# Optimization experiments

Measured on AMD Instinct MI355X. Metric: run time of the kernel, lower is better.

The kernel has to match this reference:

```python
import jax, jax.numpy as jnp
import numpy as np

N_NODES = 50000
N_EDGES = 800000
D = 128
H = 128


def setup_inputs() -> dict:
    key = jax.random.key(0)
    ks = jax.random.split(key, 8)
    s = 1.0 / np.sqrt(D)
    return {
        "x": jax.random.normal(ks[0], (N_NODES, D), dtype=jnp.float32),
        "edge_index": jax.random.randint(ks[1], (2, N_EDGES), 0, N_NODES, dtype=jnp.int64),
        "W1_l": jax.random.normal(ks[2], (D, H), dtype=jnp.float32) * s,
        "b1_l": jax.random.normal(ks[3], (H,), dtype=jnp.float32) * s,
        "W1_r": jax.random.normal(ks[4], (D, H), dtype=jnp.float32) * s,
        "W2_l": jax.random.normal(ks[5], (H, H), dtype=jnp.float32) * s,
        "b2_l": jax.random.normal(ks[6], (H,), dtype=jnp.float32) * s,
        "W2_r": jax.random.normal(ks[7], (H, H), dtype=jnp.float32) * s,
    }


def _sage_conv(x, src, dst, W_l, b_l, W_r, n_nodes):
    # mean aggregation of source features at destination nodes
    agg = jax.ops.segment_sum(x[src], dst, num_segments=n_nodes)          # [N, d]
    cnt = jax.ops.segment_sum(jnp.ones((src.shape[0],), x.dtype), dst,
                              num_segments=n_nodes)                        # [N]
    mean = agg / jnp.maximum(cnt, 1.0)[:, None]
    out = mean @ W_l + b_l + x @ W_r                                       # [N, h]
    # L2 normalize (normalize=True in SAGEConv)
    norm = jnp.linalg.norm(out, axis=-1, keepdims=True)
    return out / jnp.maximum(norm, 1e-12)


def reference(x, edge_index, W1_l, b1_l, W1_r, W2_l, b2_l, W2_r):
    src, dst = edge_index[0], edge_index[1]
    n = x.shape[0]
    h = jax.nn.relu(_sage_conv(x, src, dst, W1_l, b1_l, W1_r, n))
    h = jax.nn.relu(_sage_conv(h, src, dst, W2_l, b2_l, W2_r, n))
    return h
```

## Files before the change

kernel.cpp:

```cpp
#include <hip/hip_runtime.h>

#define N_NODES 50000
#define N_EDGES 800000
#define CAP 48

typedef __bf16 bf16_t;
typedef bf16_t bf16x8 __attribute__((ext_vector_type(8)));
typedef float f32x16 __attribute__((ext_vector_type(16)));

union Frag { float4 f4; bf16x8 h; };
union Pack8 { ushort u[8]; float4 f4; };

__device__ __forceinline__ ushort f2bf(float f) {
    unsigned u = __float_as_uint(f);
    return (ushort)((u + 0x7fffu + ((u >> 16) & 1u)) >> 16);
}
__device__ __forceinline__ float bf2f(unsigned bits) {
    return __uint_as_float(bits << 16);
}

__global__ void detect_kernel(const int* __restrict__ idx, int* __restrict__ flag) {
    int t = threadIdx.x;
    int v = idx[2 * t + 1];
    unsigned long long b = __ballot(v == 0);
    if (t == 0) *flag = (b == 0xFFFFFFFFFFFFFFFFull) ? 1 : 0;
}

__device__ __forceinline__ void load_edge(const int* __restrict__ idx, int f, int e,
                                          int& src, int& dst) {
    if (f) { src = idx[2 * e]; dst = idx[2 * N_EDGES + 2 * e]; }
    else   { src = idx[e];     dst = idx[N_EDGES + e]; }
}

__global__ __launch_bounds__(256) void prep_kernel(
        const float2* __restrict__ X, uint* __restrict__ Xb,
        int* __restrict__ deg,
        const float* __restrict__ W1l, const float* __restrict__ W1r,
        const float* __restrict__ W2l, const float* __restrict__ W2r,
        ushort* __restrict__ Bp) {
    int i = blockIdx.x * 256 + threadIdx.x;
    if (i < N_NODES * 64) {
        float2 v = X[i];
        Xb[i] = ((uint)f2bf(v.y) << 16) | (uint)f2bf(v.x);
    }
    if (i < N_NODES) deg[i] = 0;
    if (i < 8192) {
        int layer = i >> 12;
        int rec   = i & 4095;
        int t = rec >> 10;
        int s = (rec >> 6) & 15;
        int l = rec & 63;
        const float* Wl = layer ? W2l : W1l;
        const float* Wr = layer ? W2r : W1r;
        int n = t * 32 + (l & 31);
        int kb = s * 16 + (l >> 5) * 8;
        Pack8 o;
#pragma unroll
        for (int j = 0; j < 8; ++j) {
            int k = kb + j;
            float v = (k < 128) ? Wl[k * 128 + n] : Wr[(k - 128) * 128 + n];
            o.u[j] = f2bf(v);
        }
        *(float4*)(Bp + (size_t)i * 8) = o.f4;
    }
}

__global__ void bin_fixed_kernel(const int* __restrict__ idx,
                                 const int* __restrict__ flag,
                                 int* __restrict__ deg,
                                 ushort* __restrict__ esrc) {
    int e = blockIdx.x * blockDim.x + threadIdx.x;
    if (e >= N_EDGES) return;
    int f = *flag, src, dst;
    load_edge(idx, f, e, src, dst);
    int pos = atomicAdd(&deg[dst], 1);
    if (pos < CAP) esrc[dst * CAP + pos] = (ushort)src;
}

__global__ __launch_bounds__(256) void gather_mean_kernel(
        const uint2* __restrict__ X2, const int* __restrict__ deg,
        const ushort* __restrict__ esrc, uint2* __restrict__ mean2) {
    const int wave = threadIdx.x >> 6;
    const int lane = threadIdx.x & 63;
    const int node = blockIdx.x * 8 + wave * 2 + (lane >> 5);
    const int l = lane & 31;
    if (node >= N_NODES) return;
    int dg = deg[node];
    if (dg > CAP) dg = CAP;
    const ushort* es = esrc + node * CAP;

    float c0[4] = {0, 0, 0, 0}, c1[4] = {0, 0, 0, 0};
    float c2[4] = {0, 0, 0, 0}, c3[4] = {0, 0, 0, 0};
    int p = 0;
    for (; p + 3 < dg; p += 4) {
        ushort4 ss = *(const ushort4*)(es + p);
        uint2 v0 = X2[(size_t)ss.x * 32 + l];
        uint2 v1 = X2[(size_t)ss.y * 32 + l];
        uint2 v2 = X2[(size_t)ss.z * 32 + l];
        uint2 v3 = X2[(size_t)ss.w * 32 + l];
        c0[0] += bf2f(v0.x & 0xffff); c0[1] += bf2f(v0.x >> 16);
        c0[2] += bf2f(v0.y & 0xffff); c0[3] += bf2f(v0.y >> 16);
        c1[0] += bf2f(v1.x & 0xffff); c1[1] += bf2f(v1.x >> 16);
        c1[2] += bf2f(v1.y & 0xffff); c1[3] += bf2f(v1.y >> 16);
        c2[0] += bf2f(v2.x & 0xffff); c2[1] += bf2f(v2.x >> 16);
        c2[2] += bf2f(v2.y & 0xffff); c2[3] += bf2f(v2.y >> 16);
        c3[0] += bf2f(v3.x & 0xffff); c3[1] += bf2f(v3.x >> 16);
        c3[2] += bf2f(v3.y & 0xffff); c3[3] += bf2f(v3.y >> 16);
    }
    for (; p < dg; ++p) {
        uint2 v = X2[(size_t)es[p] * 32 + l];
        c0[0] += bf2f(v.x & 0xffff); c0[1] += bf2f(v.x >> 16);
        c0[2] += bf2f(v.y & 0xffff); c0[3] += bf2f(v.y >> 16);
    }
    const float inv = 1.0f / (float)max(dg, 1);
    const float m0 = (c0[0] + c1[0] + c2[0] + c3[0]) * inv;
    const float m1 = (c0[1] + c1[1] + c2[1] + c3[1]) * inv;
    const float m2 = (c0[2] + c1[2] + c2[2] + c3[2]) * inv;
    const float m3 = (c0[3] + c1[3] + c2[3] + c3[3]) * inv;
    uint2 m;
    m.x = ((uint)f2bf(m1) << 16) | (uint)f2bf(m0);
    m.y = ((uint)f2bf(m3) << 16) | (uint)f2bf(m2);
    mean2[(size_t)node * 32 + l] = m;
}

template<bool OUT_F32>
__global__ __launch_bounds__(256) void gemm_mfma_kernel(
        const ushort* __restrict__ Amean, const ushort* Aself,
        const ushort* __restrict__ Bpack, const float* __restrict__ bias,
        void* Yout) {
    __shared__ float rs[2][64];
    const int tid = threadIdx.x;
    const int w = tid >> 6, l = tid & 63;
    const int lr = l & 31, lh = l >> 5;
    const int mrow0 = blockIdx.x * 64 + (w & 1) * 32;
    const int t0 = (w >> 1) * 2;

    f32x16 acc0, acc1;
#pragma unroll
    for (int i = 0; i < 16; ++i) { acc0[i] = 0.0f; acc1[i] = 0.0f; }

#pragma unroll
    for (int s = 0; s < 16; ++s) {
        const ushort* Ab = (s < 8) ? Amean : Aself;
        Frag a, b0, b1;
        a.f4  = *(const float4*)(Ab + (size_t)(mrow0 + lr) * 128 + (s & 7) * 16 + lh * 8);
        b0.f4 = *(const float4*)(Bpack + (size_t)(((t0) * 16 + s) * 64 + l) * 8);
        b1.f4 = *(const float4*)(Bpack + (size_t)(((t0 + 1) * 16 + s) * 64 + l) * 8);
        acc0 = __builtin_amdgcn_mfma_f32_32x32x16_bf16(a.h, b0.h, acc0, 0, 0, 0);
        acc1 = __builtin_amdgcn_mfma_f32_32x32x16_bf16(a.h, b1.h, acc1, 0, 0, 0);
    }

    const float bia0 = bias[t0 * 32 + lr];
    const float bia1 = bias[t0 * 32 + 32 + lr];
    float sq[16];
#pragma unroll
    for (int r = 0; r < 16; ++r) {
        float v0 = acc0[r] + bia0;
        float v1 = acc1[r] + bia1;
        acc0[r] = v0; acc1[r] = v1;
        float s_ = v0 * v0 + v1 * v1;
        s_ += __shfl_xor(s_, 1);
        s_ += __shfl_xor(s_, 2);
        s_ += __shfl_xor(s_, 4);
        s_ += __shfl_xor(s_, 8);
        s_ += __shfl_xor(s_, 16);
        sq[r] = s_;
    }
    if (lr == 0) {
#pragma unroll
        for (int r = 0; r < 16; ++r) {
            int rowl = (w & 1) * 32 + (r & 3) + 8 * (r >> 2) + 4 * lh;
            rs[w >> 1][rowl] = sq[r];
        }
    }
    __syncthreads();
#pragma unroll
    for (int r = 0; r < 16; ++r) {
        int rowl = (w & 1) * 32 + (r & 3) + 8 * (r >> 2) + 4 * lh;
        int grow = blockIdx.x * 64 + rowl;
        float tot = rs[0][rowl] + rs[1][rowl];
        float sc = 1.0f / fmaxf(sqrtf(tot), 1e-12f);
        if (grow < N_NODES) {
            float o0 = fmaxf(acc0[r] * sc, 0.0f);
            float o1 = fmaxf(acc1[r] * sc, 0.0f);
            if (OUT_F32) {
                float* Y = (float*)Yout;
                Y[(size_t)grow * 128 + t0 * 32 + lr]      = o0;
                Y[(size_t)grow * 128 + t0 * 32 + 32 + lr] = o1;
            } else {
                ushort* Y = (ushort*)Yout;
                Y[(size_t)grow * 128 + t0 * 32 + lr]      = f2bf(o0);
                Y[(size_t)grow * 128 + t0 * 32 + 32 + lr] = f2bf(o1);
            }
        }
    }
}

extern "C" void kernel_launch(void* const* d_in, const int* in_sizes, int n_in,
                              void* d_out, int out_size, void* d_ws, size_t ws_size,
                              hipStream_t stream) {
    const float* x    = (const float*)d_in[0];
    const int*   idx  = (const int*)d_in[1];
    const float* W1l  = (const float*)d_in[2];
    const float* b1l  = (const float*)d_in[3];
    const float* W1r  = (const float*)d_in[4];
    const float* W2l  = (const float*)d_in[5];
    const float* b2l  = (const float*)d_in[6];
    const float* W2r  = (const float*)d_in[7];
    float* out = (float*)d_out;

    int*    deg   = (int*)d_ws;
    int*    flag  = deg + N_NODES;
    ushort* esrc  = (ushort*)((int*)d_ws + 50016);
    uint*   meanb = (uint*)((int*)d_ws + 1250016);
    uint*   xh    = (uint*)((int*)d_ws + 4450016);
    ushort* Bp    = (ushort*)((int*)d_ws + 7650016);

    detect_kernel<<<1, 64, 0, stream>>>(idx, flag);
    prep_kernel<<<(N_NODES * 64 + 255) / 256, 256, 0, stream>>>(
        (const float2*)x, xh, deg, W1l, W1r, W2l, W2r, Bp);
    bin_fixed_kernel<<<(N_EDGES + 255) / 256, 256, 0, stream>>>(idx, flag, deg, esrc);

    const int gb = (N_NODES + 7) / 8;
    const int mb = (N_NODES + 63) / 64;

    gather_mean_kernel<<<gb, 256, 0, stream>>>(
        (const uint2*)xh, deg, esrc, (uint2*)meanb);
    gemm_mfma_kernel<false><<<mb, 256, 0, stream>>>(
        (const ushort*)meanb, (const ushort*)xh, Bp, b1l, (void*)xh);
    gather_mean_kernel<<<gb, 256, 0, stream>>>(
        (const uint2*)xh, deg, esrc, (uint2*)meanb);
    gemm_mfma_kernel<true><<<mb, 256, 0, stream>>>(
        (const ushort*)meanb, (const ushort*)xh, Bp + 4096 * 8, b2l, (void*)out);
}
```

Baseline: 233.0 us.

## Replace global-atomic edge binning with bucketed counting sort and deeper gather unroll

Replaces the per-edge global atomicAdd binning with a bucket counting sort over 128-node buckets. A histogram pass, a single-block scan and a placement pass write packed (dst,src) pairs, then a per-bucket kernel builds the CAP-limited adjacency lists using shared-memory atomics. This targets contention and scattered traffic from global atomics on the degree array. It adds three extra kernel launches and a serial one-block scan, and it folds the layout-detection kernel into the prep kernel. The gather loop is also unrolled to 8 neighbours to keep more loads in flight.

```diff
diff --git a/kernel.cpp b/kernel.cpp
--- a/kernel.cpp
+++ b/kernel.cpp
@@ -3,6 +3,9 @@
 #define N_NODES 50000
 #define N_EDGES 800000
 #define CAP 48
+#define NBUCK 391
+#define NBK 98
+#define EPB 8192
 
 typedef __bf16 bf16_t;
 typedef bf16_t bf16x8 __attribute__((ext_vector_type(8)));
@@ -19,31 +22,22 @@
     return __uint_as_float(bits << 16);
 }
 
-__global__ void detect_kernel(const int* __restrict__ idx, int* __restrict__ flag) {
-    int t = threadIdx.x;
-    int v = idx[2 * t + 1];
-    unsigned long long b = __ballot(v == 0);
-    if (t == 0) *flag = (b == 0xFFFFFFFFFFFFFFFFull) ? 1 : 0;
-}
-
-__device__ __forceinline__ void load_edge(const int* __restrict__ idx, int f, int e,
-                                          int& src, int& dst) {
-    if (f) { src = idx[2 * e]; dst = idx[2 * N_EDGES + 2 * e]; }
-    else   { src = idx[e];     dst = idx[N_EDGES + e]; }
-}
-
 __global__ __launch_bounds__(256) void prep_kernel(
+        const int* __restrict__ idx, int* __restrict__ flag,
         const float2* __restrict__ X, uint* __restrict__ Xb,
-        int* __restrict__ deg,
         const float* __restrict__ W1l, const float* __restrict__ W1r,
         const float* __restrict__ W2l, const float* __restrict__ W2r,
         ushort* __restrict__ Bp) {
     int i = blockIdx.x * 256 + threadIdx.x;
+    if (blockIdx.x == 0 && threadIdx.x < 64) {
+        int v = idx[2 * threadIdx.x + 1];
+        unsigned long long b = __ballot(v == 0);
+        if (threadIdx.x == 0) *flag = (b == 0xFFFFFFFFFFFFFFFFull) ? 1 : 0;
+    }
     if (i < N_NODES * 64) {
         float2 v = X[i];
         Xb[i] = ((uint)f2bf(v.y) << 16) | (uint)f2bf(v.x);
     }
-    if (i < N_NODES) deg[i] = 0;
     if (i < 8192) {
         int layer = i >> 12;
         int rec   = i & 4095;
@@ -65,16 +59,89 @@
     }
 }
 
-__global__ void bin_fixed_kernel(const int* __restrict__ idx,
-                                 const int* __restrict__ flag,
-                                 int* __restrict__ deg,
-                                 ushort* __restrict__ esrc) {
-    int e = blockIdx.x * blockDim.x + threadIdx.x;
-    if (e >= N_EDGES) return;
-    int f = *flag, src, dst;
-    load_edge(idx, f, e, src, dst);
-    int pos = atomicAdd(&deg[dst], 1);
-    if (pos < CAP) esrc[dst * CAP + pos] = (ushort)src;
+__global__ __launch_bounds__(1024) void hist_kernel(
+        const int* __restrict__ idx, const int* __restrict__ flag,
+        int* __restrict__ counts) {
+    __shared__ int h[NBUCK];
+    for (int i = threadIdx.x; i < NBUCK; i += 1024) h[i] = 0;
+    __syncthreads();
+    const int f = *flag;
+    const int base = blockIdx.x * EPB;
+    const int end = min(base + EPB, N_EDGES);
+    for (int e = base + threadIdx.x; e < end; e += 1024) {
+        int dst = f ? idx[2 * N_EDGES + 2 * e] : idx[N_EDGES + e];
+        atomicAdd(&h[dst >> 7], 1);
+    }
+    __syncthreads();
+    for (int b = threadIdx.x; b < NBUCK; b += 1024)
+        counts[b * NBK + blockIdx.x] = h[b];
+}
+
+__global__ __launch_bounds__(512) void scan_kernel(int* __restrict__ counts,
+                                                   int* __restrict__ bstart) {
+    __shared__ int tot[512];
+    const int b = threadIdx.x;
+    int s = 0;
+    if (b < NBUCK)
+        for (int j = 0; j < NBK; ++j) s += counts[b * NBK + j];
+    tot[b] = (b < NBUCK) ? s : 0;
+    __syncthreads();
+    int v = tot[b];
+    for (int off = 1; off < 512; off <<= 1) {
+        int t = (b >= off) ? tot[b - off] : 0;
+        __syncthreads();
+        tot[b] += t;
+        __syncthreads();
+    }
+    const int start = tot[b] - v;
+    if (b < NBUCK) {
+        int r = start;
+        for (int j = 0; j < NBK; ++j) {
+            int c = counts[b * NBK + j];
+            counts[b * NBK + j] = r;
+            r += c;
+        }
+        bstart[b] = start;
+        if (b == NBUCK - 1) bstart[NBUCK] = start + v;
+    }
+}
+
+__global__ __launch_bounds__(1024) void place_kernel(
+        const int* __restrict__ idx, const int* __restrict__ flag,
+        const int* __restrict__ offs, uint* __restrict__ sorted) {
+    __shared__ int loc[NBUCK];
+    for (int i = threadIdx.x; i < NBUCK; i += 1024)
+        loc[i] = offs[i * NBK + blockIdx.x];
+    __syncthreads();
+    const int f = *flag;
+    const int base = blockIdx.x * EPB;
+    const int end = min(base + EPB, N_EDGES);
+    for (int e = base + threadIdx.x; e < end; e += 1024) {
+        int src, dst;
+        if (f) { src = idx[2 * e]; dst = idx[2 * N_EDGES + 2 * e]; }
+        else   { src = idx[e];     dst = idx[N_EDGES + e]; }
+        int pos = atomicAdd(&loc[dst >> 7], 1);
+        sorted[pos] = ((uint)dst << 16) | (uint)src;
+    }
+}
+
+__global__ __launch_bounds__(256) void bin_kernel(
+        const uint* __restrict__ sorted, const int* __restrict__ bstart,
+        int* __restrict__ deg, ushort* __restrict__ esrc) {
+    __shared__ int cnt[128];
+    const int b = blockIdx.x;
+    if (threadIdx.x < 128) cnt[threadIdx.x] = 0;
+    __syncthreads();
+    const int s = bstart[b], e = bstart[b + 1];
+    for (int i = s + threadIdx.x; i < e; i += 256) {
+        uint r = sorted[i];
+        int dst = r >> 16, src = r & 0xffff;
+        int pos = atomicAdd(&cnt[dst & 127], 1);
+        if (pos < CAP) esrc[dst * CAP + pos] = (ushort)src;
+    }
+    __syncthreads();
+    const int node = b * 128 + threadIdx.x;
+    if (threadIdx.x < 128 && node < N_NODES) deg[node] = cnt[threadIdx.x];
 }
 
 __global__ __launch_bounds__(256) void gather_mean_kernel(
@@ -92,12 +159,17 @@
     float c0[4] = {0, 0, 0, 0}, c1[4] = {0, 0, 0, 0};
     float c2[4] = {0, 0, 0, 0}, c3[4] = {0, 0, 0, 0};
     int p = 0;
-    for (; p + 3 < dg; p += 4) {
-        ushort4 ss = *(const ushort4*)(es + p);
-        uint2 v0 = X2[(size_t)ss.x * 32 + l];
-        uint2 v1 = X2[(size_t)ss.y * 32 + l];
-        uint2 v2 = X2[(size_t)ss.z * 32 + l];
-        uint2 v3 = X2[(size_t)ss.w * 32 + l];
+    for (; p + 7 < dg; p += 8) {
+        ushort4 sa = *(const ushort4*)(es + p);
+        ushort4 sb = *(const ushort4*)(es + p + 4);
+        uint2 v0 = X2[(size_t)sa.x * 32 + l];
+        uint2 v1 = X2[(size_t)sa.y * 32 + l];
+        uint2 v2 = X2[(size_t)sa.z * 32 + l];
+        uint2 v3 = X2[(size_t)sa.w * 32 + l];
+        uint2 v4 = X2[(size_t)sb.x * 32 + l];
+        uint2 v5 = X2[(size_t)sb.y * 32 + l];
+        uint2 v6 = X2[(size_t)sb.z * 32 + l];
+        uint2 v7 = X2[(size_t)sb.w * 32 + l];
         c0[0] += bf2f(v0.x & 0xffff); c0[1] += bf2f(v0.x >> 16);
         c0[2] += bf2f(v0.y & 0xffff); c0[3] += bf2f(v0.y >> 16);
         c1[0] += bf2f(v1.x & 0xffff); c1[1] += bf2f(v1.x >> 16);
@@ -106,6 +178,14 @@
         c2[2] += bf2f(v2.y & 0xffff); c2[3] += bf2f(v2.y >> 16);
         c3[0] += bf2f(v3.x & 0xffff); c3[1] += bf2f(v3.x >> 16);
         c3[2] += bf2f(v3.y & 0xffff); c3[3] += bf2f(v3.y >> 16);
+        c0[0] += bf2f(v4.x & 0xffff); c0[1] += bf2f(v4.x >> 16);
+        c0[2] += bf2f(v4.y & 0xffff); c0[3] += bf2f(v4.y >> 16);
+        c1[0] += bf2f(v5.x & 0xffff); c1[1] += bf2f(v5.x >> 16);
+        c1[2] += bf2f(v5.y & 0xffff); c1[3] += bf2f(v5.y >> 16);
+        c2[0] += bf2f(v6.x & 0xffff); c2[1] += bf2f(v6.x >> 16);
+        c2[2] += bf2f(v6.y & 0xffff); c2[3] += bf2f(v6.y >> 16);
+        c3[0] += bf2f(v7.x & 0xffff); c3[1] += bf2f(v7.x >> 16);
+        c3[2] += bf2f(v7.y & 0xffff); c3[3] += bf2f(v7.y >> 16);
     }
     for (; p < dg; ++p) {
         uint2 v = X2[(size_t)es[p] * 32 + l];
@@ -209,17 +289,22 @@
     const float* W2r  = (const float*)d_in[7];
     float* out = (float*)d_out;
 
-    int*    deg   = (int*)d_ws;
-    int*    flag  = deg + N_NODES;
-    ushort* esrc  = (ushort*)((int*)d_ws + 50016);
-    uint*   meanb = (uint*)((int*)d_ws + 1250016);
-    uint*   xh    = (uint*)((int*)d_ws + 4450016);
-    ushort* Bp    = (ushort*)((int*)d_ws + 7650016);
-
-    detect_kernel<<<1, 64, 0, stream>>>(idx, flag);
+    int*    deg    = (int*)d_ws;
+    int*    flag   = deg + N_NODES;
+    ushort* esrc   = (ushort*)((int*)d_ws + 50016);
+    uint*   meanb  = (uint*)((int*)d_ws + 1250016);
+    int*    counts = (int*)meanb;
+    int*    bstart = (int*)((int*)d_ws + 1290016);
+    uint*   sorted = (uint*)((int*)d_ws + 1300000);
+    uint*   xh     = (uint*)((int*)d_ws + 4450016);
+    ushort* Bp     = (ushort*)((int*)d_ws + 7650016);
+
     prep_kernel<<<(N_NODES * 64 + 255) / 256, 256, 0, stream>>>(
-        (const float2*)x, xh, deg, W1l, W1r, W2l, W2r, Bp);
-    bin_fixed_kernel<<<(N_EDGES + 255) / 256, 256, 0, stream>>>(idx, flag, deg, esrc);
+        idx, flag, (const float2*)x, xh, W1l, W1r, W2l, W2r, Bp);
+    hist_kernel<<<NBK, 1024, 0, stream>>>(idx, flag, counts);
+    scan_kernel<<<1, 512, 0, stream>>>(counts, bstart);
+    place_kernel<<<NBK, 1024, 0, stream>>>(idx, flag, counts, sorted);
+    bin_kernel<<<NBUCK, 256, 0, stream>>>(sorted, bstart, deg, esrc);
 
     const int gb = (N_NODES + 7) / 8;
     const int mb = (N_NODES + 63) / 64;
```

After: 234.3 us. No clear change (+0.6%).
